# Performance work log

Hardware: AMD Instinct MI355X
Metric: run time of the kernel (lower is better)

Reference implementation:

```python
import jax, jax.numpy as jnp
import numpy as np

B, T, C, H = 4, 2048, 1024, 16
D = C // H  # head dim = 64

def setup_inputs() -> dict:
    key = jax.random.key(0)
    k1, k2, k3 = jax.random.split(key, 3)
    x = jax.random.normal(k1, (B, T, C), dtype=jnp.float32)
    w_attn = jax.random.normal(k2, (C, 3 * C), dtype=jnp.float32) * 0.02
    b_attn = jnp.zeros((3 * C,), dtype=jnp.float32)
    w_proj = jax.random.normal(k3, (C, C), dtype=jnp.float32) * 0.02
    b_proj = jnp.zeros((C,), dtype=jnp.float32)
    return {"x": x, "w_attn": w_attn, "b_attn": b_attn, "w_proj": w_proj, "b_proj": b_proj}

def reference(x, w_attn, b_attn, w_proj, b_proj):
    Bx, Tx, Cx = x.shape
    qkv = x @ w_attn + b_attn  # [B, T, 3C]
    q, k, v = jnp.split(qkv, 3, axis=2)
    # [B, H, T, D]
    q = q.reshape(Bx, Tx, H, D).swapaxes(1, 2)
    k = k.reshape(Bx, Tx, H, D).swapaxes(1, 2)
    v = v.reshape(Bx, Tx, H, D).swapaxes(1, 2)
    scale = 1.0 / jnp.sqrt(jnp.asarray(D, dtype=x.dtype))
    att = jnp.einsum('bhqd,bhkd->bhqk', q, k) * scale  # [B, H, T, T]
    causal = jnp.tril(jnp.ones((Tx, Tx), dtype=bool))
    att = jnp.where(causal[None, None], att, -jnp.inf)
    att = jax.nn.softmax(att, axis=-1)
    y = jnp.einsum('bhqk,bhkd->bhqd', att, v)  # [B, H, T, D]
    y = y.swapaxes(1, 2).reshape(Bx, Tx, Cx)
    return y @ w_proj + b_proj
```

## Files before the change

kernel.cpp:

```cpp
#include <hip/hip_runtime.h>
#include <hip/hip_bf16.h>
#include <cstdint>

#define B_ 4
#define T_ 2048
#define C_ 1024
#define H_ 16
#define D_ 64

#define BM 256
#define BN 128
#define BK 64
#define ASZ (BM * BK)
#define BSZ (BN * BK)

typedef __bf16 bf16x8 __attribute__((ext_vector_type(8)));
typedef float f32x4 __attribute__((ext_vector_type(4)));

static __device__ __forceinline__ float bf2f(unsigned short u) {
    union { unsigned int i; float f; } w;
    w.i = ((unsigned int)u) << 16;
    return w.f;
}
static __device__ __forceinline__ unsigned short f2bf(float f) {
    unsigned int i = __float_as_uint(f);
    unsigned int r = (i + 0x7FFFu + ((i >> 16) & 1u)) >> 16;
    return (unsigned short)r;
}
static __device__ __forceinline__ float exp2_fast(float x) {
    float r;
    asm("v_exp_f32 %0, %1" : "=v"(r) : "v"(x));
    return r;
}

static __device__ __forceinline__ void gl_lds16(const unsigned short* g,
                                                unsigned short* l) {
    __builtin_amdgcn_global_load_lds(
        (const __attribute__((address_space(1))) unsigned int*)g,
        (__attribute__((address_space(3))) unsigned int*)l, 16, 0, 0);
}

__global__ __launch_bounds__(256)
void convert_f32_bf16(const float* __restrict__ in,
                      unsigned short* __restrict__ out, int n) {
    int i = (blockIdx.x * 256 + threadIdx.x) * 8;
    if (i < n) {
        float4 a = *(const float4*)(in + i);
        float4 b = *(const float4*)(in + i + 4);
        ushort4 s0 = {f2bf(a.x), f2bf(a.y), f2bf(a.z), f2bf(a.w)};
        ushort4 s1 = {f2bf(b.x), f2bf(b.y), f2bf(b.z), f2bf(b.w)};
        *(ushort4*)(out + i) = s0;
        *(ushort4*)(out + i + 4) = s1;
    }
}

__global__ void transpose_f32_bf16(const float* __restrict__ in,
                                   unsigned short* __restrict__ out,
                                   int R, int Cc) {
    __shared__ unsigned short tile[32][33];
    int c0 = blockIdx.x * 32;
    int r0 = blockIdx.y * 32;
    int tx = threadIdx.x, ty = threadIdx.y;
    #pragma unroll
    for (int i = ty; i < 32; i += 8)
        tile[i][tx] = f2bf(in[(size_t)(r0 + i) * Cc + c0 + tx]);
    __syncthreads();
    #pragma unroll
    for (int i = ty; i < 32; i += 8)
        out[(size_t)(c0 + i) * R + r0 + tx] = tile[tx][i];
}

__global__ __launch_bounds__(512)
void gemm_qkv(const unsigned short* __restrict__ A,
              const unsigned short* __restrict__ Bt,
              const float* __restrict__ bias,
              unsigned short* __restrict__ qkv,
              unsigned short* __restrict__ vt,
              int M, float qscale) {
    const int K = C_;
    __shared__ __align__(16) unsigned short Ab[3 * ASZ];
    __shared__ __align__(16) unsigned short Bb[3 * BSZ];

    int tid = threadIdx.x;
    int nwg = gridDim.x * gridDim.y;
    int flat = blockIdx.y * gridDim.x + blockIdx.x;
    int swz = (flat & 7) * (nwg >> 3) + (flat >> 3);
    int bx = swz % gridDim.x;
    int by = swz / gridDim.x;
    int row0 = by * BM;
    int col0 = bx * BN;

    int wave = tid >> 6, lane = tid & 63;
    int wm = wave >> 1, wn = wave & 1;
    int m16 = lane & 15, quad = lane >> 4;

    int arow = tid >> 3;
    int achk = (tid & 7) ^ (arow & 7);
    const unsigned short* aps = A + (size_t)(row0 + arow) * K + achk * 8;
    const unsigned short* bps = Bt + (size_t)(col0 + arow) * K + achk * 8;
    unsigned short* adst = Ab + tid * 8;
    unsigned short* bdst = Bb + tid * 8;

    f32x4 acc[4][4];
    #pragma unroll
    for (int i = 0; i < 4; ++i)
        #pragma unroll
        for (int j = 0; j < 4; ++j)
            acc[i][j] = (f32x4){0.f, 0.f, 0.f, 0.f};

    auto STAGE = [&](int koff, int oa, int ob) {
        #pragma unroll
        for (int l = 0; l < 4; ++l)
            gl_lds16(aps + (size_t)(l * 64) * K + koff, adst + oa + l * 4096);
        #pragma unroll
        for (int l = 0; l < 2; ++l)
            gl_lds16(bps + (size_t)(l * 64) * K + koff, bdst + ob + l * 4096);
    };

    int rbA = wm * 64 + m16;
    int rbB = wn * 64 + m16;
    int pc0 = ((0 + quad) ^ (m16 & 7)) * 8;
    int pc1 = ((4 + quad) ^ (m16 & 7)) * 8;

    auto PHASE = [&](int oa, int ob, int pc) {
        bf16x8 af[4], bfr[4];
        #pragma unroll
        for (int i = 0; i < 4; ++i)
            af[i] = *(const bf16x8*)(Ab + oa + (rbA + i * 16) * 64 + pc);
        #pragma unroll
        for (int j = 0; j < 4; ++j)
            bfr[j] = *(const bf16x8*)(Bb + ob + (rbB + j * 16) * 64 + pc);
        __builtin_amdgcn_s_setprio(1);
        #pragma unroll
        for (int i = 0; i < 4; ++i)
            #pragma unroll
            for (int j = 0; j < 4; ++j)
                acc[i][j] = __builtin_amdgcn_mfma_f32_16x16x32_bf16(
                    af[i], bfr[j], acc[i][j], 0, 0, 0);
        __builtin_amdgcn_s_setprio(0);
    };

    STAGE(0, 0, 0);
    STAGE(BK, ASZ, BSZ);
    asm volatile("s_waitcnt vmcnt(6)" ::: "memory");
    __builtin_amdgcn_s_barrier();

    int oa0 = 0, oa1 = ASZ, oa2 = 2 * ASZ;
    int ob0 = 0, ob1 = BSZ, ob2 = 2 * BSZ;
    const int NT = K / BK;
    for (int t = 0; t < NT; ++t) {
        if (t + 2 < NT) STAGE((t + 2) * BK, oa2, ob2);
        PHASE(oa0, ob0, pc0);
        PHASE(oa0, ob0, pc1);
        if (t + 1 < NT) {
            if (t + 2 < NT) asm volatile("s_waitcnt vmcnt(6)" ::: "memory");
            else            asm volatile("s_waitcnt vmcnt(0)" ::: "memory");
            __builtin_amdgcn_s_barrier();
        }
        int x;
        x = oa0; oa0 = oa1; oa1 = oa2; oa2 = x;
        x = ob0; ob0 = ob1; ob1 = ob2; ob2 = x;
    }
    __syncthreads();

    float bv[4];
    #pragma unroll
    for (int j = 0; j < 4; ++j)
        bv[j] = bias[col0 + wn * 64 + j * 16 + m16];

    unsigned short* wbuf = Ab + wave * 2048;
    bool isV = (col0 >= 2 * C_);
    float sc = (col0 < C_) ? qscale : 1.0f;
    int b_loc = row0 >> 11;
    int trow0 = (row0 & 2047) + wm * 64;

    #pragma unroll
    for (int sub = 0; sub < 4; ++sub) {
        int i0 = (sub >> 1) << 1;
        int j0 = (sub & 1) << 1;
        #pragma unroll
        for (int jj = 0; jj < 2; ++jj) {
            #pragma unroll
            for (int ii = 0; ii < 2; ++ii) {
                #pragma unroll
                for (int rr = 0; rr < 4; ++rr) {
                    int rl = ii * 16 + quad * 4 + rr;
                    int cl = jj * 16 + m16;
                    unsigned short hv =
                        f2bf((acc[i0 + ii][j0 + jj][rr] + bv[j0 + jj]) * sc);
                    if (!isV) wbuf[rl * 40 + cl] = hv;
                    else      wbuf[cl * 40 + rl] = hv;
                }
            }
        }
        __builtin_amdgcn_sched_barrier(0);
        if (!isV) {
            #pragma unroll
            for (int it = 0; it < 4; ++it) {
                int rl = it * 8 + (lane >> 3);
                int cc = (lane & 7) << 2;
                uint2 v2 = *(const uint2*)&wbuf[rl * 40 + cc];
                int rowg = row0 + wm * 64 + i0 * 16 + rl;
                int colg = col0 + wn * 64 + j0 * 16 + cc;
                *(uint2*)&qkv[(size_t)rowg * (2 * C_) + colg] = v2;
            }
        } else {
            int head = ((col0 - 2 * C_) + wn * 64) >> 6;
            unsigned short* vtb =
                vt + (size_t)((b_loc * H_ + head) * 64) * T_;
            #pragma unroll
            for (int it = 0; it < 4; ++it) {
                int dsub = it * 8 + (lane >> 3);
                int tc = (lane & 7) << 2;
                uint2 v2 = *(const uint2*)&wbuf[dsub * 40 + tc];
                int d = j0 * 16 + dsub;
                int tg = trow0 + i0 * 16 + tc;
                *(uint2*)&vtb[(size_t)d * T_ + tg] = v2;
            }
        }
        __builtin_amdgcn_sched_barrier(0);
    }
}

__global__ __launch_bounds__(512)
void gemm_out(const unsigned short* __restrict__ A, int lda,
              const unsigned short* __restrict__ Bt,
              const float* __restrict__ bias,
              float* __restrict__ Cmat,
              int M, int N, int K) {
    __shared__ __align__(16) unsigned short Ab[3 * ASZ];
    __shared__ __align__(16) unsigned short Bb[3 * BSZ];

    int tid = threadIdx.x;
    int nwg = gridDim.x * gridDim.y;
    int flat = blockIdx.y * gridDim.x + blockIdx.x;
    int swz = (flat & 7) * (nwg >> 3) + (flat >> 3);
    int bx = swz % gridDim.x;
    int by = swz / gridDim.x;
    int row0 = by * BM;
    int col0 = bx * BN;

    int wave = tid >> 6, lane = tid & 63;
    int wm = wave >> 1, wn = wave & 1;
    int m16 = lane & 15, quad = lane >> 4;

    int arow = tid >> 3;
    int achk = (tid & 7) ^ (arow & 7);
    const unsigned short* aps = A + (size_t)(row0 + arow) * lda + achk * 8;
    const unsigned short* bps = Bt + (size_t)(col0 + arow) * K + achk * 8;
    unsigned short* adst = Ab + tid * 8;
    unsigned short* bdst = Bb + tid * 8;

    f32x4 acc[4][4];
    #pragma unroll
    for (int i = 0; i < 4; ++i)
        #pragma unroll
        for (int j = 0; j < 4; ++j)
            acc[i][j] = (f32x4){0.f, 0.f, 0.f, 0.f};

    auto STAGE = [&](int koff, int oa, int ob) {
        #pragma unroll
        for (int l = 0; l < 4; ++l)
            gl_lds16(aps + (size_t)(l * 64) * lda + koff, adst + oa + l * 4096);
        #pragma unroll
        for (int l = 0; l < 2; ++l)
            gl_lds16(bps + (size_t)(l * 64) * K + koff, bdst + ob + l * 4096);
    };

    int rbA = wm * 64 + m16;
    int rbB = wn * 64 + m16;
    int pc0 = ((0 + quad) ^ (m16 & 7)) * 8;
    int pc1 = ((4 + quad) ^ (m16 & 7)) * 8;

    auto PHASE = [&](int oa, int ob, int pc) {
        bf16x8 af[4], bfr[4];
        #pragma unroll
        for (int i = 0; i < 4; ++i)
            af[i] = *(const bf16x8*)(Ab + oa + (rbA + i * 16) * 64 + pc);
        #pragma unroll
        for (int j = 0; j < 4; ++j)
            bfr[j] = *(const bf16x8*)(Bb + ob + (rbB + j * 16) * 64 + pc);
        __builtin_amdgcn_s_setprio(1);
        #pragma unroll
        for (int i = 0; i < 4; ++i)
            #pragma unroll
            for (int j = 0; j < 4; ++j)
                acc[i][j] = __builtin_amdgcn_mfma_f32_16x16x32_bf16(
                    af[i], bfr[j], acc[i][j], 0, 0, 0);
        __builtin_amdgcn_s_setprio(0);
    };

    STAGE(0, 0, 0);
    STAGE(BK, ASZ, BSZ);
    asm volatile("s_waitcnt vmcnt(6)" ::: "memory");
    __builtin_amdgcn_s_barrier();

    int oa0 = 0, oa1 = ASZ, oa2 = 2 * ASZ;
    int ob0 = 0, ob1 = BSZ, ob2 = 2 * BSZ;
    const int NT = C_ / BK;
    for (int t = 0; t < NT; ++t) {
        if (t + 2 < NT) STAGE((t + 2) * BK, oa2, ob2);
        PHASE(oa0, ob0, pc0);
        PHASE(oa0, ob0, pc1);
        if (t + 1 < NT) {
            if (t + 2 < NT) asm volatile("s_waitcnt vmcnt(6)" ::: "memory");
            else            asm volatile("s_waitcnt vmcnt(0)" ::: "memory");
            __builtin_amdgcn_s_barrier();
        }
        int x;
        x = oa0; oa0 = oa1; oa1 = oa2; oa2 = x;
        x = ob0; ob0 = ob1; ob1 = ob2; ob2 = x;
    }

    #pragma unroll
    for (int j = 0; j < 4; ++j) {
        int col = col0 + wn * 64 + j * 16 + m16;
        float bvv = bias[col];
        #pragma unroll
        for (int i = 0; i < 4; ++i) {
            int row = row0 + wm * 64 + i * 16 + quad * 4;
            #pragma unroll
            for (int rr = 0; rr < 4; ++rr)
                Cmat[(size_t)(row + rr) * N + col] = acc[i][j][rr] + bvv;
        }
    }
}

__global__ __launch_bounds__(256)
void attn_mfma(unsigned short* __restrict__ qkv,
               const unsigned short* __restrict__ vt) {
    __shared__ __align__(16) unsigned short Ks[2][64][80];
    __shared__ __align__(16) unsigned short Vs[2][64][80];
    __shared__ __align__(16) unsigned short Pb[4][16][72];

    int bh = blockIdx.x;
    int b = bh >> 4, h = bh & 15;
    int qb = (T_ / 64 - 1) - blockIdx.y;
    int tid = threadIdx.x;
    int wave = tid >> 6;
    int lane = tid & 63;
    int m16 = lane & 15, quad = lane >> 4;

    const size_t rs = 2 * C_;
    unsigned short* base = qkv + (size_t)b * T_ * rs + h * 64;
    const unsigned short* kb0 = base + C_;
    const unsigned short* vtb = vt + (size_t)bh * 64 * T_;

    int qrow = qb * 64 + wave * 16 + m16;
    const unsigned short* qp = base + (size_t)qrow * rs;
    bf16x8 qf0 = *(const bf16x8*)(qp + quad * 8);
    bf16x8 qf1 = *(const bf16x8*)(qp + 32 + quad * 8);

    f32x4 o[4];
    #pragma unroll
    for (int dt = 0; dt < 4; ++dt) o[dt] = (f32x4){0.f, 0.f, 0.f, 0.f};
    float lrow[4] = {0.f, 0.f, 0.f, 0.f};

    int qg0 = qb * 64 + wave * 16 + quad * 4;
    int ntiles = qb + 1;

    int kkey = tid >> 3, kdc = (tid & 7) << 3;
    int vd   = tid >> 3, vkc = (tid & 7) << 3;

    uint4 ra  = *(const uint4*)(kb0 + (size_t)kkey * rs + kdc);
    uint4 rb  = *(const uint4*)(kb0 + (size_t)(kkey + 32) * rs + kdc);
    uint4 rva = *(const uint4*)(vtb + (size_t)vd * T_ + vkc);
    uint4 rvb = *(const uint4*)(vtb + (size_t)(vd + 32) * T_ + vkc);
    *(uint4*)&Ks[0][kkey][kdc]      = ra;
    *(uint4*)&Ks[0][kkey + 32][kdc] = rb;
    *(uint4*)&Vs[0][vd][vkc]        = rva;
    *(uint4*)&Vs[0][vd + 32][vkc]   = rvb;
    if (ntiles > 1) {
        const unsigned short* kn = kb0 + (size_t)64 * rs;
        ra  = *(const uint4*)(kn + (size_t)kkey * rs + kdc);
        rb  = *(const uint4*)(kn + (size_t)(kkey + 32) * rs + kdc);
        rva = *(const uint4*)(vtb + (size_t)vd * T_ + 64 + vkc);
        rvb = *(const uint4*)(vtb + (size_t)(vd + 32) * T_ + 64 + vkc);
    }
    __syncthreads();

    for (int kt = 0; kt < ntiles; ++kt) {
        int cur = kt & 1;

        f32x4 s[4];
        #pragma unroll
        for (int st = 0; st < 4; ++st) {
            f32x4 acc = (f32x4){0.f, 0.f, 0.f, 0.f};
            bf16x8 k0 = *(const bf16x8*)&Ks[cur][st * 16 + m16][quad * 8];
            bf16x8 k1 = *(const bf16x8*)&Ks[cur][st * 16 + m16][32 + quad * 8];
            acc = __builtin_amdgcn_mfma_f32_16x16x32_bf16(qf0, k0, acc, 0, 0, 0);
            acc = __builtin_amdgcn_mfma_f32_16x16x32_bf16(qf1, k1, acc, 0, 0, 0);
            s[st] = acc;
        }

        if (kt == qb) {
            #pragma unroll
            for (int st = 0; st < 4; ++st) {
                int kg = kt * 64 + st * 16 + m16;
                #pragma unroll
                for (int r = 0; r < 4; ++r)
                    if (kg > qg0 + r) s[st][r] = -1.0e30f;
            }
        }

        #pragma unroll
        for (int st = 0; st < 4; ++st) {
            #pragma unroll
            for (int r = 0; r < 4; ++r) {
                float p = exp2_fast(s[st][r]);
                lrow[r] += p;
                Pb[wave][quad * 4 + r][st * 16 + m16] = f2bf(p);
            }
        }
        __builtin_amdgcn_sched_barrier(0);

        #pragma unroll
        for (int s2 = 0; s2 < 2; ++s2) {
            bf16x8 pa = *(const bf16x8*)&Pb[wave][m16][s2 * 32 + quad * 8];
            #pragma unroll
            for (int dt = 0; dt < 4; ++dt) {
                bf16x8 vv = *(const bf16x8*)&Vs[cur][dt * 16 + m16][s2 * 32 + quad * 8];
                o[dt] = __builtin_amdgcn_mfma_f32_16x16x32_bf16(pa, vv, o[dt], 0, 0, 0);
            }
        }

        if (kt + 1 < ntiles) {
            int nxt = (kt + 1) & 1;
            *(uint4*)&Ks[nxt][kkey][kdc]      = ra;
            *(uint4*)&Ks[nxt][kkey + 32][kdc] = rb;
            *(uint4*)&Vs[nxt][vd][vkc]        = rva;
            *(uint4*)&Vs[nxt][vd + 32][vkc]   = rvb;
            if (kt + 2 < ntiles) {
                const unsigned short* kn = kb0 + (size_t)((kt + 2) * 64) * rs;
                ra  = *(const uint4*)(kn + (size_t)kkey * rs + kdc);
                rb  = *(const uint4*)(kn + (size_t)(kkey + 32) * rs + kdc);
                rva = *(const uint4*)(vtb + (size_t)vd * T_ + (kt + 2) * 64 + vkc);
                rvb = *(const uint4*)(vtb + (size_t)(vd + 32) * T_ + (kt + 2) * 64 + vkc);
            }
        }
        __syncthreads();
    }

    float lf[4];
    #pragma unroll
    for (int r = 0; r < 4; ++r) lf[r] = lrow[r];
    #pragma unroll
    for (int off = 1; off <= 8; off <<= 1)
        #pragma unroll
        for (int r = 0; r < 4; ++r)
            lf[r] += __shfl_xor(lf[r], off);

    #pragma unroll
    for (int r = 0; r < 4; ++r) {
        float inv = 1.0f / lf[r];
        unsigned short* op = base + (size_t)(qg0 + r) * rs;
        #pragma unroll
        for (int dt = 0; dt < 4; ++dt)
            op[dt * 16 + m16] = f2bf(o[dt][r] * inv);
    }
}

extern "C" void kernel_launch(void* const* d_in, const int* in_sizes, int n_in,
                              void* d_out, int out_size, void* d_ws, size_t ws_size,
                              hipStream_t stream) {
    const float* x      = (const float*)d_in[0];
    const float* w_attn = (const float*)d_in[1];
    const float* b_attn = (const float*)d_in[2];
    const float* w_proj = (const float*)d_in[3];
    const float* b_proj = (const float*)d_in[4];
    float* out = (float*)d_out;

    unsigned short* ws = (unsigned short*)d_ws;
    unsigned short* xb       = ws;
    unsigned short* w_attn_t = xb + (size_t)B_ * T_ * C_;
    unsigned short* w_proj_t = w_attn_t + (size_t)3 * C_ * C_;
    unsigned short* qkv      = w_proj_t + (size_t)C_ * C_;

    const size_t fixed_hw = (size_t)B_ * T_ * C_ + 4 * (size_t)C_ * C_;
    const size_t per_b_hw = (size_t)T_ * 2 * C_ + (size_t)H_ * 64 * T_;
    int bstep = (ws_size >= (fixed_hw + (size_t)B_ * per_b_hw) * sizeof(unsigned short))
                ? B_ : 1;

    int nx = B_ * T_ * C_;
    convert_f32_bf16<<<nx / 2048, 256, 0, stream>>>(x, xb, nx);
    transpose_f32_bf16<<<dim3(3 * C_ / 32, C_ / 32), dim3(32, 8), 0, stream>>>(
        w_attn, w_attn_t, C_, 3 * C_);
    transpose_f32_bf16<<<dim3(C_ / 32, C_ / 32), dim3(32, 8), 0, stream>>>(
        w_proj, w_proj_t, C_, C_);

    const float QSCALE = 0.125f * 1.44269504088896341f;

    for (int b0 = 0; b0 < B_; b0 += bstep) {
        int M = bstep * T_;
        const unsigned short* xbb = xb + (size_t)b0 * T_ * C_;
        float* ob = out + (size_t)b0 * T_ * C_;
        unsigned short* vt = qkv + (size_t)bstep * T_ * 2 * C_;

        gemm_qkv<<<dim3(3 * C_ / BN, M / BM), 512, 0, stream>>>(
            xbb, w_attn_t, b_attn, qkv, vt, M, QSCALE);

        attn_mfma<<<dim3(bstep * H_, T_ / 64), 256, 0, stream>>>(qkv, vt);

        gemm_out<<<dim3(C_ / BN, M / BM), 512, 0, stream>>>(
            qkv, 2 * C_, w_proj_t, b_proj, out + (size_t)b0 * T_ * C_, M, C_, C_);
    }
}
```

Before: 266.0 us.

## Interleave half-tile global loads with MFMA phases using ping-pong barrier scheduling

Both GEMM kernels' main loops are restructured so each K-tile's global-to-LDS prefetch is split into two halves. Each half is issued between the LDS fragment reads and the MFMA block of one phase. Explicit s_barrier, lgkmcnt waits and sched_barrier fences separate memory and compute phases, in the style of a ping-pong schedule, so the load and MFMA work of different waves overlap. This adds more barriers per iteration in exchange for a more evenly spread memory traffic. An unused local variable in the host loop is also removed.

```diff
diff --git a/kernel.cpp b/kernel.cpp
--- a/kernel.cpp
+++ b/kernel.cpp
@@ -108,13 +108,16 @@
         for (int j = 0; j < 4; ++j)
             acc[i][j] = (f32x4){0.f, 0.f, 0.f, 0.f};
 
-    auto STAGE = [&](int koff, int oa, int ob) {
-        #pragma unroll
-        for (int l = 0; l < 4; ++l)
-            gl_lds16(aps + (size_t)(l * 64) * K + koff, adst + oa + l * 4096);
-        #pragma unroll
-        for (int l = 0; l < 2; ++l)
-            gl_lds16(bps + (size_t)(l * 64) * K + koff, bdst + ob + l * 4096);
+    auto STAGE_H = [&](int koff, int oa, int ob, int half) {
+        if (half == 0) {
+            gl_lds16(aps + (size_t)(0 * 64) * K + koff, adst + oa + 0 * 4096);
+            gl_lds16(aps + (size_t)(1 * 64) * K + koff, adst + oa + 1 * 4096);
+            gl_lds16(bps + (size_t)(0 * 64) * K + koff, bdst + ob + 0 * 4096);
+        } else {
+            gl_lds16(aps + (size_t)(2 * 64) * K + koff, adst + oa + 2 * 4096);
+            gl_lds16(aps + (size_t)(3 * 64) * K + koff, adst + oa + 3 * 4096);
+            gl_lds16(bps + (size_t)(1 * 64) * K + koff, bdst + ob + 1 * 4096);
+        }
     };
 
     int rbA = wm * 64 + m16;
@@ -122,26 +125,10 @@
     int pc0 = ((0 + quad) ^ (m16 & 7)) * 8;
     int pc1 = ((4 + quad) ^ (m16 & 7)) * 8;
 
-    auto PHASE = [&](int oa, int ob, int pc) {
-        bf16x8 af[4], bfr[4];
-        #pragma unroll
-        for (int i = 0; i < 4; ++i)
-            af[i] = *(const bf16x8*)(Ab + oa + (rbA + i * 16) * 64 + pc);
-        #pragma unroll
-        for (int j = 0; j < 4; ++j)
-            bfr[j] = *(const bf16x8*)(Bb + ob + (rbB + j * 16) * 64 + pc);
-        __builtin_amdgcn_s_setprio(1);
-        #pragma unroll
-        for (int i = 0; i < 4; ++i)
-            #pragma unroll
-            for (int j = 0; j < 4; ++j)
-                acc[i][j] = __builtin_amdgcn_mfma_f32_16x16x32_bf16(
-                    af[i], bfr[j], acc[i][j], 0, 0, 0);
-        __builtin_amdgcn_s_setprio(0);
-    };
-
-    STAGE(0, 0, 0);
-    STAGE(BK, ASZ, BSZ);
+    STAGE_H(0, 0, 0, 0);
+    STAGE_H(0, 0, 0, 1);
+    STAGE_H(BK, ASZ, BSZ, 0);
+    STAGE_H(BK, ASZ, BSZ, 1);
     asm volatile("s_waitcnt vmcnt(6)" ::: "memory");
     __builtin_amdgcn_s_barrier();
 
@@ -149,13 +136,56 @@
     int ob0 = 0, ob1 = BSZ, ob2 = 2 * BSZ;
     const int NT = K / BK;
     for (int t = 0; t < NT; ++t) {
-        if (t + 2 < NT) STAGE((t + 2) * BK, oa2, ob2);
-        PHASE(oa0, ob0, pc0);
-        PHASE(oa0, ob0, pc1);
-        if (t + 1 < NT) {
-            if (t + 2 < NT) asm volatile("s_waitcnt vmcnt(6)" ::: "memory");
-            else            asm volatile("s_waitcnt vmcnt(0)" ::: "memory");
+        bool st = (t + 2 < NT);
+        {
+            bf16x8 af[4], bfr[4];
+            #pragma unroll
+            for (int i = 0; i < 4; ++i)
+                af[i] = *(const bf16x8*)(Ab + oa0 + (rbA + i * 16) * 64 + pc0);
+            #pragma unroll
+            for (int j = 0; j < 4; ++j)
+                bfr[j] = *(const bf16x8*)(Bb + ob0 + (rbB + j * 16) * 64 + pc0);
+            if (st) STAGE_H((t + 2) * BK, oa2, ob2, 0);
             __builtin_amdgcn_s_barrier();
+            asm volatile("s_waitcnt lgkmcnt(0)" ::: "memory");
+            __builtin_amdgcn_sched_barrier(0);
+            __builtin_amdgcn_s_setprio(1);
+            #pragma unroll
+            for (int i = 0; i < 4; ++i)
+                #pragma unroll
+                for (int j = 0; j < 4; ++j)
+                    acc[i][j] = __builtin_amdgcn_mfma_f32_16x16x32_bf16(
+                        af[i], bfr[j], acc[i][j], 0, 0, 0);
+            __builtin_amdgcn_s_setprio(0);
+            __builtin_amdgcn_sched_barrier(0);
+            __builtin_amdgcn_s_barrier();
+        }
+        {
+            bf16x8 af[4], bfr[4];
+            #pragma unroll
+            for (int i = 0; i < 4; ++i)
+                af[i] = *(const bf16x8*)(Ab + oa0 + (rbA + i * 16) * 64 + pc1);
+            #pragma unroll
+            for (int j = 0; j < 4; ++j)
+                bfr[j] = *(const bf16x8*)(Bb + ob0 + (rbB + j * 16) * 64 + pc1);
+            if (st) STAGE_H((t + 2) * BK, oa2, ob2, 1);
+            if (t + 1 < NT) {
+                if (st) asm volatile("s_waitcnt vmcnt(6)" ::: "memory");
+                else    asm volatile("s_waitcnt vmcnt(0)" ::: "memory");
+            }
+            __builtin_amdgcn_s_barrier();
+            asm volatile("s_waitcnt lgkmcnt(0)" ::: "memory");
+            __builtin_amdgcn_sched_barrier(0);
+            __builtin_amdgcn_s_setprio(1);
+            #pragma unroll
+            for (int i = 0; i < 4; ++i)
+                #pragma unroll
+                for (int j = 0; j < 4; ++j)
+                    acc[i][j] = __builtin_amdgcn_mfma_f32_16x16x32_bf16(
+                        af[i], bfr[j], acc[i][j], 0, 0, 0);
+            __builtin_amdgcn_s_setprio(0);
+            __builtin_amdgcn_sched_barrier(0);
+            if (t + 1 < NT) __builtin_amdgcn_s_barrier();
         }
         int x;
         x = oa0; oa0 = oa1; oa1 = oa2; oa2 = x;
@@ -258,13 +288,16 @@
         for (int j = 0; j < 4; ++j)
             acc[i][j] = (f32x4){0.f, 0.f, 0.f, 0.f};
 
-    auto STAGE = [&](int koff, int oa, int ob) {
-        #pragma unroll
-        for (int l = 0; l < 4; ++l)
-            gl_lds16(aps + (size_t)(l * 64) * lda + koff, adst + oa + l * 4096);
-        #pragma unroll
-        for (int l = 0; l < 2; ++l)
-            gl_lds16(bps + (size_t)(l * 64) * K + koff, bdst + ob + l * 4096);
+    auto STAGE_H = [&](int koff, int oa, int ob, int half) {
+        if (half == 0) {
+            gl_lds16(aps + (size_t)(0 * 64) * lda + koff, adst + oa + 0 * 4096);
+            gl_lds16(aps + (size_t)(1 * 64) * lda + koff, adst + oa + 1 * 4096);
+            gl_lds16(bps + (size_t)(0 * 64) * K + koff, bdst + ob + 0 * 4096);
+        } else {
+            gl_lds16(aps + (size_t)(2 * 64) * lda + koff, adst + oa + 2 * 4096);
+            gl_lds16(aps + (size_t)(3 * 64) * lda + koff, adst + oa + 3 * 4096);
+            gl_lds16(bps + (size_t)(1 * 64) * K + koff, bdst + ob + 1 * 4096);
+        }
     };
 
     int rbA = wm * 64 + m16;
@@ -272,26 +305,10 @@
     int pc0 = ((0 + quad) ^ (m16 & 7)) * 8;
     int pc1 = ((4 + quad) ^ (m16 & 7)) * 8;
 
-    auto PHASE = [&](int oa, int ob, int pc) {
-        bf16x8 af[4], bfr[4];
-        #pragma unroll
-        for (int i = 0; i < 4; ++i)
-            af[i] = *(const bf16x8*)(Ab + oa + (rbA + i * 16) * 64 + pc);
-        #pragma unroll
-        for (int j = 0; j < 4; ++j)
-            bfr[j] = *(const bf16x8*)(Bb + ob + (rbB + j * 16) * 64 + pc);
-        __builtin_amdgcn_s_setprio(1);
-        #pragma unroll
-        for (int i = 0; i < 4; ++i)
-            #pragma unroll
-            for (int j = 0; j < 4; ++j)
-                acc[i][j] = __builtin_amdgcn_mfma_f32_16x16x32_bf16(
-                    af[i], bfr[j], acc[i][j], 0, 0, 0);
-        __builtin_amdgcn_s_setprio(0);
-    };
-
-    STAGE(0, 0, 0);
-    STAGE(BK, ASZ, BSZ);
+    STAGE_H(0, 0, 0, 0);
+    STAGE_H(0, 0, 0, 1);
+    STAGE_H(BK, ASZ, BSZ, 0);
+    STAGE_H(BK, ASZ, BSZ, 1);
     asm volatile("s_waitcnt vmcnt(6)" ::: "memory");
     __builtin_amdgcn_s_barrier();
 
@@ -299,13 +316,56 @@
     int ob0 = 0, ob1 = BSZ, ob2 = 2 * BSZ;
     const int NT = C_ / BK;
     for (int t = 0; t < NT; ++t) {
-        if (t + 2 < NT) STAGE((t + 2) * BK, oa2, ob2);
-        PHASE(oa0, ob0, pc0);
-        PHASE(oa0, ob0, pc1);
-        if (t + 1 < NT) {
-            if (t + 2 < NT) asm volatile("s_waitcnt vmcnt(6)" ::: "memory");
-            else            asm volatile("s_waitcnt vmcnt(0)" ::: "memory");
+        bool st = (t + 2 < NT);
+        {
+            bf16x8 af[4], bfr[4];
+            #pragma unroll
+            for (int i = 0; i < 4; ++i)
+                af[i] = *(const bf16x8*)(Ab + oa0 + (rbA + i * 16) * 64 + pc0);
+            #pragma unroll
+            for (int j = 0; j < 4; ++j)
+                bfr[j] = *(const bf16x8*)(Bb + ob0 + (rbB + j * 16) * 64 + pc0);
+            if (st) STAGE_H((t + 2) * BK, oa2, ob2, 0);
             __builtin_amdgcn_s_barrier();
+            asm volatile("s_waitcnt lgkmcnt(0)" ::: "memory");
+            __builtin_amdgcn_sched_barrier(0);
+            __builtin_amdgcn_s_setprio(1);
+            #pragma unroll
+            for (int i = 0; i < 4; ++i)
+                #pragma unroll
+                for (int j = 0; j < 4; ++j)
+                    acc[i][j] = __builtin_amdgcn_mfma_f32_16x16x32_bf16(
+                        af[i], bfr[j], acc[i][j], 0, 0, 0);
+            __builtin_amdgcn_s_setprio(0);
+            __builtin_amdgcn_sched_barrier(0);
+            __builtin_amdgcn_s_barrier();
+        }
+        {
+            bf16x8 af[4], bfr[4];
+            #pragma unroll
+            for (int i = 0; i < 4; ++i)
+                af[i] = *(const bf16x8*)(Ab + oa0 + (rbA + i * 16) * 64 + pc1);
+            #pragma unroll
+            for (int j = 0; j < 4; ++j)
+                bfr[j] = *(const bf16x8*)(Bb + ob0 + (rbB + j * 16) * 64 + pc1);
+            if (st) STAGE_H((t + 2) * BK, oa2, ob2, 1);
+            if (t + 1 < NT) {
+                if (st) asm volatile("s_waitcnt vmcnt(6)" ::: "memory");
+                else    asm volatile("s_waitcnt vmcnt(0)" ::: "memory");
+            }
+            __builtin_amdgcn_s_barrier();
+            asm volatile("s_waitcnt lgkmcnt(0)" ::: "memory");
+            __builtin_amdgcn_sched_barrier(0);
+            __builtin_amdgcn_s_setprio(1);
+            #pragma unroll
+            for (int i = 0; i < 4; ++i)
+                #pragma unroll
+                for (int j = 0; j < 4; ++j)
+                    acc[i][j] = __builtin_amdgcn_mfma_f32_16x16x32_bf16(
+                        af[i], bfr[j], acc[i][j], 0, 0, 0);
+            __builtin_amdgcn_s_setprio(0);
+            __builtin_amdgcn_sched_barrier(0);
+            if (t + 1 < NT) __builtin_amdgcn_s_barrier();
         }
         int x;
         x = oa0; oa0 = oa1; oa1 = oa2; oa2 = x;
@@ -493,7 +553,6 @@
     for (int b0 = 0; b0 < B_; b0 += bstep) {
         int M = bstep * T_;
         const unsigned short* xbb = xb + (size_t)b0 * T_ * C_;
-        float* ob = out + (size_t)b0 * T_ * C_;
         unsigned short* vt = qkv + (size_t)bstep * T_ * 2 * C_;
 
         gemm_qkv<<<dim3(3 * C_ / BN, M / BM), 512, 0, stream>>>(
```

After: 267.5 us. Within noise of the previous version (+0.5%).
